# Performance work log

Measured on AMD Instinct MI355X. Metric: run time of the kernel, lower is better.

## Reference

```python
import jax, jax.numpy as jnp
import numpy as np

B, S, H = 256, 4096, 128

def setup_inputs() -> dict:
    key = jax.random.key(0)
    k1, k2 = jax.random.split(key)
    encoder_outputs = jax.random.normal(k1, (B, S, H), dtype=jnp.float32)
    attention_weights = jax.random.normal(k2, (H, 1), dtype=jnp.float32)
    return {"encoder_outputs": encoder_outputs, "attention_weights": attention_weights}

def reference(encoder_outputs, attention_weights):
    # scores: [B, S] = tanh(x) @ w  (w: [H,1] -> squeeze)
    energy = jnp.tanh(encoder_outputs)
    scores = jnp.einsum('bsh,h->bs', energy, attention_weights[:, 0])
    attn = jax.nn.softmax(scores, axis=1)            # softmax over sequence dim
    # context: [B, H] = sum_s attn[b,s] * x[b,s,:]
    context = jnp.einsum('bsh,bs->bh', encoder_outputs, attn)
    return context
```

## Files before the change

kernel.cpp:

```cpp
#include <hip/hip_runtime.h>
#include <math.h>

#define BB 256
#define SS 4096
#define HH 128
#define SPLIT 8
#define SCHUNK (SS / SPLIT)
#define NW 4
#define NTHREADS (NW * 64)

__device__ __forceinline__ float fast_tanh(float x) {
    return 1.0f - 2.0f / (1.0f + __expf(2.0f * x));
}

__global__ __launch_bounds__(NTHREADS) void attn_pass1(
    const float* __restrict__ x, const float* __restrict__ w,
    float* __restrict__ pm, float* __restrict__ pl, float* __restrict__ pc)
{
    const int b     = blockIdx.x / SPLIT;
    const int chunk = blockIdx.x % SPLIT;
    const int wave  = threadIdx.x >> 6;
    const int lane  = threadIdx.x & 63;

    const float2* __restrict__ x2 =
        (const float2*)x + (size_t)b * (SS * (HH / 2)) + (size_t)(chunk * SCHUNK) * (HH / 2);
    const float2 wv = ((const float2*)w)[lane];

    float m = -INFINITY, l = 0.f, c0 = 0.f, c1 = 0.f;

    for (int s = wave; s < SCHUNK; s += NW) {
        float2 v = x2[(size_t)s * (HH / 2) + lane];
        float t = fast_tanh(v.x) * wv.x + fast_tanh(v.y) * wv.y;
        #pragma unroll
        for (int off = 1; off < 64; off <<= 1)
            t += __shfl_xor(t, off, 64);
        float nm = fmaxf(m, t);
        float sc = __expf(m - nm);
        float p  = __expf(t - nm);
        l  = l  * sc + p;
        c0 = c0 * sc + p * v.x;
        c1 = c1 * sc + p * v.y;
        m  = nm;
    }

    __shared__ float sm[NW], sl[NW], scx[NW][HH];
    if (lane == 0) { sm[wave] = m; sl[wave] = l; }
    scx[wave][2 * lane]     = c0;
    scx[wave][2 * lane + 1] = c1;
    __syncthreads();

    if (wave == 0) {
        float M = sm[0];
        #pragma unroll
        for (int i = 1; i < NW; i++) M = fmaxf(M, sm[i]);
        float L = 0.f, C0 = 0.f, C1 = 0.f;
        #pragma unroll
        for (int i = 0; i < NW; i++) {
            float e = __expf(sm[i] - M);
            L  += sl[i] * e;
            C0 += scx[i][2 * lane]     * e;
            C1 += scx[i][2 * lane + 1] * e;
        }
        const int idx = b * SPLIT + chunk;
        if (lane == 0) { pm[idx] = M; pl[idx] = L; }
        pc[(size_t)idx * HH + 2 * lane]     = C0;
        pc[(size_t)idx * HH + 2 * lane + 1] = C1;
    }
}

__global__ __launch_bounds__(64) void attn_pass2(
    const float* __restrict__ pm, const float* __restrict__ pl,
    const float* __restrict__ pc, float* __restrict__ out)
{
    const int b    = blockIdx.x;
    const int lane = threadIdx.x;

    float M = -INFINITY;
    #pragma unroll
    for (int i = 0; i < SPLIT; i++) M = fmaxf(M, pm[b * SPLIT + i]);

    float L = 0.f, C0 = 0.f, C1 = 0.f;
    #pragma unroll
    for (int i = 0; i < SPLIT; i++) {
        float e = __expf(pm[b * SPLIT + i] - M);
        L  += pl[b * SPLIT + i] * e;
        C0 += pc[(size_t)(b * SPLIT + i) * HH + 2 * lane]     * e;
        C1 += pc[(size_t)(b * SPLIT + i) * HH + 2 * lane + 1] * e;
    }
    out[b * HH + 2 * lane]     = C0 / L;
    out[b * HH + 2 * lane + 1] = C1 / L;
}

extern "C" void kernel_launch(void* const* d_in, const int* in_sizes, int n_in,
                              void* d_out, int out_size, void* d_ws, size_t ws_size,
                              hipStream_t stream) {
    const float* x = (const float*)d_in[0];
    const float* w = (const float*)d_in[1];
    float* out = (float*)d_out;

    float* pm = (float*)d_ws;
    float* pl = pm + BB * SPLIT;
    float* pc = pl + BB * SPLIT;

    attn_pass1<<<BB * SPLIT, NTHREADS, 0, stream>>>(x, w, pm, pl, pc);
    attn_pass2<<<BB, 64, 0, stream>>>(pm, pl, pc, out);
}
```

Measured before the change: 698.0 us.

## Process two sequence rows per wave with float4 loads and lazy rescaling

Result: faster. 682.2 us (-2.3%).

```diff
diff --git a/kernel.cpp b/kernel.cpp
--- a/kernel.cpp
+++ b/kernel.cpp
@@ -21,41 +21,49 @@
     const int chunk = blockIdx.x % SPLIT;
     const int wave  = threadIdx.x >> 6;
     const int lane  = threadIdx.x & 63;
+    const int half  = lane >> 5;
+    const int hl    = lane & 31;
 
-    const float2* __restrict__ x2 =
-        (const float2*)x + (size_t)b * (SS * (HH / 2)) + (size_t)(chunk * SCHUNK) * (HH / 2);
-    const float2 wv = ((const float2*)w)[lane];
+    const float4* __restrict__ x4 =
+        (const float4*)x + (size_t)b * (SS * (HH / 4)) + (size_t)(chunk * SCHUNK) * (HH / 4);
+    const float4 wv = ((const float4*)w)[hl];
 
-    float m = -INFINITY, l = 0.f, c0 = 0.f, c1 = 0.f;
+    float m = -INFINITY, l = 0.f, c0 = 0.f, c1 = 0.f, c2 = 0.f, c3 = 0.f;
 
-    for (int s = wave; s < SCHUNK; s += NW) {
-        float2 v = x2[(size_t)s * (HH / 2) + lane];
-        float t = fast_tanh(v.x) * wv.x + fast_tanh(v.y) * wv.y;
+    #pragma unroll 2
+    for (int p = wave; p < SCHUNK / 2; p += NW) {
+        float4 v = x4[(size_t)p * 64 + lane];
+        float t = fast_tanh(v.x) * wv.x + fast_tanh(v.y) * wv.y
+                + fast_tanh(v.z) * wv.z + fast_tanh(v.w) * wv.w;
         #pragma unroll
-        for (int off = 1; off < 64; off <<= 1)
+        for (int off = 1; off < 32; off <<= 1)
             t += __shfl_xor(t, off, 64);
-        float nm = fmaxf(m, t);
-        float sc = __expf(m - nm);
-        float p  = __expf(t - nm);
-        l  = l  * sc + p;
-        c0 = c0 * sc + p * v.x;
-        c1 = c1 * sc + p * v.y;
-        m  = nm;
+        if (t > m) {
+            float sc = __expf(m - t);
+            l *= sc; c0 *= sc; c1 *= sc; c2 *= sc; c3 *= sc;
+            m = t;
+        }
+        float pp = __expf(t - m);
+        l  += pp;
+        c0 += pp * v.x; c1 += pp * v.y; c2 += pp * v.z; c3 += pp * v.w;
     }
 
-    __shared__ float sm[NW], sl[NW], scx[NW][HH];
-    if (lane == 0) { sm[wave] = m; sl[wave] = l; }
-    scx[wave][2 * lane]     = c0;
-    scx[wave][2 * lane + 1] = c1;
+    __shared__ float sm[NW * 2], sl[NW * 2], scx[NW * 2][HH];
+    const int part = wave * 2 + half;
+    if (hl == 0) { sm[part] = m; sl[part] = l; }
+    scx[part][4 * hl + 0] = c0;
+    scx[part][4 * hl + 1] = c1;
+    scx[part][4 * hl + 2] = c2;
+    scx[part][4 * hl + 3] = c3;
     __syncthreads();
 
     if (wave == 0) {
         float M = sm[0];
         #pragma unroll
-        for (int i = 1; i < NW; i++) M = fmaxf(M, sm[i]);
+        for (int i = 1; i < NW * 2; i++) M = fmaxf(M, sm[i]);
         float L = 0.f, C0 = 0.f, C1 = 0.f;
         #pragma unroll
-        for (int i = 0; i < NW; i++) {
+        for (int i = 0; i < NW * 2; i++) {
             float e = __expf(sm[i] - M);
             L  += sl[i] * e;
             C0 += scx[i][2 * lane]     * e;
```
